# Performance work log

Measured on AMD Instinct MI355X. Metric: run time of the kernel, lower is better.

Reference implementation:

```python
import jax, jax.numpy as jnp
import numpy as np

B = 4096       # batch
D = 256        # num_features
H = 512        # proposal_hidden_units
K = 10         # mixture_components
C = 64         # context_units
L = 4          # proposal_residual_blocks
S = 10         # num_importance_samples (call default)
HEAD = 3 * K + C
LOG2PI = float(np.log(2.0 * np.pi))


def setup_inputs() -> dict:
    key = jax.random.key(0)
    ks = jax.random.split(key, 10)
    x = jax.random.normal(ks[0], (B, D), jnp.float32)
    observed_mask = (jax.random.uniform(ks[1], (B, D)) < 0.5).astype(jnp.float32)
    s_in = 1.0 / np.sqrt(2 * D)
    s_h = 1.0 / np.sqrt(H)
    W_in = (jax.random.normal(ks[2], (2 * D, H), jnp.float32) * s_in)
    b_in = jnp.zeros((H,), jnp.float32)
    W1 = jax.random.normal(ks[3], (L, H, H), jnp.float32) * s_h
    b1 = jnp.zeros((L, H), jnp.float32)
    W2 = jax.random.normal(ks[4], (L, H, H), jnp.float32) * s_h
    b2 = jnp.zeros((L, H), jnp.float32)
    W_fin = jax.random.normal(ks[5], (H, D * HEAD), jnp.float32) * s_h
    b_fin = jnp.zeros((D * HEAD,), jnp.float32)
    return {
        "x": x, "observed_mask": observed_mask,
        "W_in": W_in, "b_in": b_in,
        "W1": W1, "b1": b1, "W2": W2, "b2": b2,
        "W_fin": W_fin, "b_fin": b_fin,
        "num_importance_samples": S,
    }


def _proposal_params(x_o, observed_mask, W_in, b_in, W1, b1, W2, b2, W_fin, b_fin):
    # Residual MLP proposal network on [x_o, observed_mask].
    h = jnp.concatenate([x_o, observed_mask], axis=-1) @ W_in + b_in  # [B, H]
    for l in range(L):
        r = jax.nn.relu(h) @ W1[l] + b1[l]
        r = jax.nn.relu(r) @ W2[l] + b2[l]
        h = h + r
    out = (h @ W_fin + b_fin).reshape(h.shape[0], D, HEAD)  # [B, D, 3K+C]
    logits = out[..., :K]
    means = out[..., K:2 * K]
    scales = jax.nn.softplus(out[..., 2 * K:3 * K]) + 1e-3
    return logits, means, scales


def reference(x, observed_mask, W_in, b_in, W1, b1, W2, b2, W_fin, b_fin,
              num_importance_samples):
    query = 1.0 - observed_mask
    x_o = x * observed_mask
    x_u = x * query

    logits, means, scales = _proposal_params(
        x_o, observed_mask, W_in, b_in, W1, b1, W2, b2, W_fin, b_fin)

    # Per-feature mixture-of-Gaussians log-likelihood of x_u, masked by query.
    log_w = jax.nn.log_softmax(logits, axis=-1)               # [B, D, K]
    z = (x_u[..., None] - means) / scales
    comp_ll = -0.5 * z * z - jnp.log(scales) - 0.5 * LOG2PI   # [B, D, K]
    proposal_ll = jax.scipy.special.logsumexp(log_w + comp_ll, axis=-1) * query

    # Samples (stop_gradient in the original).
    skey = jax.random.key(1234)
    kc, kn = jax.random.split(skey)
    comp = jax.random.categorical(kc, logits, axis=-1,
                                  shape=(num_importance_samples,) + logits.shape[:2])  # [S, B, D]
    mu = jnp.take_along_axis(means[None], comp[..., None], axis=-1)[..., 0]    # [S, B, D]
    sg = jnp.take_along_axis(scales[None], comp[..., None], axis=-1)[..., 0]   # [S, B, D]
    eps = jax.random.normal(kn, comp.shape, jnp.float32)
    samples = mu + sg * eps                                   # [S, B, D]
    samples = jnp.transpose(samples, (1, 0, 2))               # [B, S, D]
    samples = jax.lax.stop_gradient(samples) * query[:, None, :]
    # call() multiplies by query twice (before and after selected_features block)
    proposal_samples = samples * query[:, None, :]

    proposal_mean = jnp.sum(jax.nn.softmax(logits, axis=-1) * means, axis=-1) * query
    proposal_mean = proposal_mean * query  # second masking, as in call()

    return proposal_ll, proposal_samples, proposal_mean
```

## Files before the change

kernel.cpp:

```cpp
#include <hip/hip_runtime.h>
#include <cstdint>

#define B 4096
#define D 256
#define H 512
#define K 10
#define NL 4
#define S 10
#define NOUT 30
#define HEADW 94
#define ND (B*D)
#define NFIN 7680
#define NLOG 2560
#define NMS  5120

typedef __bf16 bf16x8 __attribute__((ext_vector_type(8)));
typedef float  f32x16 __attribute__((ext_vector_type(16)));

__host__ __device__ inline void threefry2x32(uint32_t k0, uint32_t k1,
                                             uint32_t x0, uint32_t x1,
                                             uint32_t& o0, uint32_t& o1) {
  uint32_t ks2 = k0 ^ k1 ^ 0x1BD11BDAu;
#define TF_ROT(x, r) (((x) << (r)) | ((x) >> (32 - (r))))
#define TF_RND(r) { x0 += x1; x1 = TF_ROT(x1, r); x1 ^= x0; }
  x0 += k0; x1 += k1;
  TF_RND(13) TF_RND(15) TF_RND(26) TF_RND(6)
  x0 += k1; x1 += ks2 + 1u;
  TF_RND(17) TF_RND(29) TF_RND(16) TF_RND(24)
  x0 += ks2; x1 += k0 + 2u;
  TF_RND(13) TF_RND(15) TF_RND(26) TF_RND(6)
  x0 += k0; x1 += k1 + 3u;
  TF_RND(17) TF_RND(29) TF_RND(16) TF_RND(24)
  x0 += k1; x1 += ks2 + 4u;
  TF_RND(13) TF_RND(15) TF_RND(26) TF_RND(6)
  x0 += ks2; x1 += k0 + 5u;
  o0 = x0; o1 = x1;
#undef TF_RND
#undef TF_ROT
}

__device__ __forceinline__ uint32_t rb32(uint32_t k0, uint32_t k1, uint32_t idx) {
  uint32_t a, b;
  threefry2x32(k0, k1, 0u, idx, a, b);
  return a ^ b;
}

__device__ __forceinline__ float u01_from_bits(uint32_t bits) {
  return __uint_as_float((bits >> 9) | 0x3f800000u) - 1.0f;
}

__device__ __forceinline__ float erfinv_f32(float x) {
  float w = -log1pf(-x * x);
  float p;
  if (w < 5.0f) {
    w = w - 2.5f;
    p = 2.81022636e-08f;
    p = fmaf(p, w, 3.43273939e-07f);
    p = fmaf(p, w, -3.5233877e-06f);
    p = fmaf(p, w, -4.39150654e-06f);
    p = fmaf(p, w, 0.00021858087f);
    p = fmaf(p, w, -0.00125372503f);
    p = fmaf(p, w, -0.00417768164f);
    p = fmaf(p, w, 0.246640727f);
    p = fmaf(p, w, 1.50140941f);
  } else {
    w = sqrtf(w) - 3.0f;
    p = -0.000200214257f;
    p = fmaf(p, w, 0.000100950558f);
    p = fmaf(p, w, 0.00134934322f);
    p = fmaf(p, w, -0.00367342844f);
    p = fmaf(p, w, 0.00573950773f);
    p = fmaf(p, w, -0.0076224613f);
    p = fmaf(p, w, 0.00943887047f);
    p = fmaf(p, w, 1.00167406f);
    p = fmaf(p, w, 2.83297682f);
  }
  return p * x;
}

__device__ __forceinline__ unsigned short bf16_rne(float x) {
  uint32_t u = __float_as_uint(x);
  uint32_t r = u + 0x7fffu + ((u >> 16) & 1u);
  return (unsigned short)(r >> 16);
}

__device__ __forceinline__ void split2(float x, short& hi, short& lo) {
  unsigned short hb = bf16_rne(x);
  float hf = __uint_as_float((uint32_t)hb << 16);
  hi = (short)hb;
  lo = (short)bf16_rne(x - hf);
}

__device__ __forceinline__ void gload16(const void* g, void* l) {
  __builtin_amdgcn_global_load_lds(
      (const __attribute__((address_space(1))) void*)g,
      (__attribute__((address_space(3))) void*)l, 16, 0, 0);
}

template <int ROWS>
__device__ __forceinline__ void stage_region(const short* __restrict__ g,
                                             short* l, int wid, int lane) {
#pragma unroll
  for (int c = wid; c < ROWS / 16; c += 4) {
    const short* gp = g + (size_t)(c * 16 + (lane >> 2)) * 512 + (lane & 3) * 8;
    gload16(gp, l + c * 512);
  }
}

__global__ __launch_bounds__(256) void prep_kernel(const float* __restrict__ x,
                                                   const float* __restrict__ mask,
                                                   float* __restrict__ xcat) {
  int i = blockIdx.x * 256 + threadIdx.x;
  if (i >= B * 2 * D) return;
  int b = i >> 9, c = i & 511;
  float v = (c < D) ? x[b * D + c] * mask[b * D + c] : mask[b * D + (c - D)];
  xcat[i] = v;
}

__global__ __launch_bounds__(256) void wgatherL(const float* __restrict__ Wf,
                                                float* __restrict__ wsgL) {
  int c = blockIdx.x * 256 + threadIdx.x;
  int k = blockIdx.y;
  int dd = c / K, j = c - dd * K;
  wsgL[(size_t)k * NLOG + c] = Wf[(size_t)k * (D * HEADW) + dd * HEADW + j];
}

__global__ __launch_bounds__(256) void wsplit_ms(const float* __restrict__ Wf,
                                                 short* __restrict__ whi,
                                                 short* __restrict__ wlo) {
  __shared__ float tile[32][33];
  int n0 = blockIdx.x * 32, k0 = blockIdx.y * 32;
  int tx = threadIdx.x & 31, ty = threadIdx.x >> 5;
#pragma unroll
  for (int r = 0; r < 4; ++r) {
    int k = k0 + ty + r * 8;
    int n = n0 + tx;
    int dd = n / 20, j = n - dd * 20;
    tile[ty + r * 8][tx] = Wf[(size_t)k * (D * HEADW) + dd * HEADW + 10 + j];
  }
  __syncthreads();
#pragma unroll
  for (int r = 0; r < 4; ++r) {
    int n = n0 + ty + r * 8;
    int k = k0 + tx;
    float v = tile[tx][ty + r * 8];
    short hb, lb;
    split2(v, hb, lb);
    whi[(size_t)n * 512 + k] = hb;
    wlo[(size_t)n * 512 + k] = lb;
  }
}

template <int RELU, int RES>
__global__ __launch_bounds__(128) void gemm_trunk(const float* __restrict__ A,
                                                  const float* __restrict__ W,
                                                  const float* __restrict__ bias,
                                                  const float* res, float* C) {
  __shared__ float As[32 * 68];
  __shared__ float Ws[32 * 64];
  const int tid = threadIdx.x;
  const int lane = tid & 63, wid = tid >> 6;
  const int tx = tid & 15, ty = tid >> 4;
  const int bm = blockIdx.y * 64, bn = blockIdx.x * 64;
  const int ls = tid & 7, lm = tid >> 3;

  float acc[8][4] = {};

  for (int k0 = 0; k0 < H; k0 += 32) {
#pragma unroll
    for (int c = wid; c < 8; c += 2) {
      gload16(W + (size_t)(k0 + c * 4 + (lane >> 4)) * H + bn + (lane & 15) * 4,
              Ws + c * 256 + lane * 4);
    }
#pragma unroll
    for (int r = 0; r < 4; ++r) {
      int m = lm + 16 * r;
      float4 f = *(const float4*)(A + (size_t)(bm + m) * H + k0 + 4 * ls);
      if (RELU) {
        f.x = fmaxf(f.x, 0.0f); f.y = fmaxf(f.y, 0.0f);
        f.z = fmaxf(f.z, 0.0f); f.w = fmaxf(f.w, 0.0f);
      }
      As[(4 * ls + 0) * 68 + m] = f.x;
      As[(4 * ls + 1) * 68 + m] = f.y;
      As[(4 * ls + 2) * 68 + m] = f.z;
      As[(4 * ls + 3) * 68 + m] = f.w;
    }
    __syncthreads();
#pragma unroll
    for (int kk = 0; kk < 32; ++kk) {
      float a[8], b[4];
      *(float4*)(a + 0) = *(const float4*)(As + kk * 68 + ty * 8);
      *(float4*)(a + 4) = *(const float4*)(As + kk * 68 + ty * 8 + 4);
      *(float4*)(b + 0) = *(const float4*)(Ws + kk * 64 + tx * 4);
#pragma unroll
      for (int i = 0; i < 8; ++i)
#pragma unroll
        for (int j = 0; j < 4; ++j) acc[i][j] = fmaf(a[i], b[j], acc[i][j]);
    }
    __syncthreads();
  }
#pragma unroll
  for (int i = 0; i < 8; ++i) {
    int row = bm + ty * 8 + i;
#pragma unroll
    for (int j = 0; j < 4; ++j) {
      int col = bn + tx * 4 + j;
      float v = acc[i][j] + bias[col];
      if (RES) v = res[(size_t)row * H + col] + v;
      C[(size_t)row * H + col] = v;
    }
  }
}

__global__ __launch_bounds__(256) void gemm_logits(const float* __restrict__ A,
                                                   const float* __restrict__ Wg,
                                                   const float* __restrict__ bf,
                                                   float* __restrict__ headout) {
  __shared__ float As[32 * 136];
  __shared__ float Ws[32 * 128];
  const int tid = threadIdx.x;
  const int lane = tid & 63, wid = tid >> 6;
  const int tx = tid & 15, ty = tid >> 4;
  const int bm = blockIdx.y * 128, bn = blockIdx.x * 128;
  const int ls = tid & 7, lm = tid >> 3;

  float acc[8][8] = {};

  for (int k0 = 0; k0 < H; k0 += 32) {
#pragma unroll
    for (int c = wid; c < 16; c += 4) {
      gload16(Wg + (size_t)(k0 + c * 2 + (lane >> 5)) * NLOG + bn + (lane & 31) * 4,
              Ws + c * 256 + lane * 4);
    }
#pragma unroll
    for (int r = 0; r < 4; ++r) {
      int m = lm + 32 * r;
      float4 f = *(const float4*)(A + (size_t)(bm + m) * H + k0 + 4 * ls);
      As[(4 * ls + 0) * 136 + m] = f.x;
      As[(4 * ls + 1) * 136 + m] = f.y;
      As[(4 * ls + 2) * 136 + m] = f.z;
      As[(4 * ls + 3) * 136 + m] = f.w;
    }
    __syncthreads();
#pragma unroll
    for (int kk = 0; kk < 32; ++kk) {
      float a[8], b[8];
      *(float4*)(a + 0) = *(const float4*)(As + kk * 136 + ty * 8);
      *(float4*)(a + 4) = *(const float4*)(As + kk * 136 + ty * 8 + 4);
      *(float4*)(b + 0) = *(const float4*)(Ws + kk * 128 + tx * 8);
      *(float4*)(b + 4) = *(const float4*)(Ws + kk * 128 + tx * 8 + 4);
#pragma unroll
      for (int i = 0; i < 8; ++i)
#pragma unroll
        for (int j = 0; j < 8; ++j) acc[i][j] = fmaf(a[i], b[j], acc[i][j]);
    }
    __syncthreads();
  }
#pragma unroll
  for (int i = 0; i < 8; ++i) {
    int row = bm + ty * 8 + i;
#pragma unroll
    for (int j = 0; j < 8; ++j) {
      int c = bn + tx * 8 + j;
      int dd = c / K, jj = c - dd * K;
      float v = acc[i][j] + bf[dd * HEADW + jj];
      headout[(size_t)row * NFIN + dd * NOUT + jj] = v;
    }
  }
}

__global__ __launch_bounds__(256) void gemm_ms(const float* __restrict__ A,
                                               const short* __restrict__ Bh,
                                               const short* __restrict__ Bl,
                                               const float* __restrict__ bf,
                                               float* __restrict__ headout) {
  __shared__ short lds[4 * 128 * 32];
  const int tid = threadIdx.x;
  const int lane = tid & 63, wid = tid >> 6;
  const int wm = wid >> 1, wn = wid & 1;
  const int bm = blockIdx.y * 128, bn = blockIdx.x * 128;
  const int ls = tid & 7, lm = tid >> 3;

  short* ldsAh = lds;
  short* ldsAl = lds + 4096;
  short* ldsBh = lds + 8192;
  short* ldsBl = lds + 12288;

  const short* gBh = Bh + (size_t)bn * 512;
  const short* gBl = Bl + (size_t)bn * 512;

  f32x16 acc[2][2];
#pragma unroll
  for (int mt = 0; mt < 2; ++mt)
#pragma unroll
    for (int nt = 0; nt < 2; ++nt)
#pragma unroll
      for (int i = 0; i < 16; ++i) acc[mt][nt][i] = 0.0f;

  for (int k0 = 0; k0 < 512; k0 += 32) {
    stage_region<128>(gBh + k0, ldsBh, wid, lane);
    stage_region<128>(gBl + k0, ldsBl, wid, lane);
#pragma unroll
    for (int r = 0; r < 4; ++r) {
      int m = lm + 32 * r;
      float4 f = *(const float4*)(A + (size_t)(bm + m) * H + k0 + 4 * ls);
      short4 h4, l4;
      split2(f.x, h4.x, l4.x); split2(f.y, h4.y, l4.y);
      split2(f.z, h4.z, l4.z); split2(f.w, h4.w, l4.w);
      *(short4*)(ldsAh + m * 32 + 4 * ls) = h4;
      *(short4*)(ldsAl + m * 32 + 4 * ls) = l4;
    }
    __syncthreads();
#pragma unroll
    for (int sub = 0; sub < 2; ++sub) {
      bf16x8 ah[2], al[2], bh[2], bl[2];
#pragma unroll
      for (int mt = 0; mt < 2; ++mt) {
        int r = wm * 64 + mt * 32 + (lane & 31);
        int off = r * 32 + sub * 16 + (lane >> 5) * 8;
        ah[mt] = *(const bf16x8*)(ldsAh + off);
        al[mt] = *(const bf16x8*)(ldsAl + off);
      }
#pragma unroll
      for (int nt = 0; nt < 2; ++nt) {
        int r = wn * 64 + nt * 32 + (lane & 31);
        int off = r * 32 + sub * 16 + (lane >> 5) * 8;
        bh[nt] = *(const bf16x8*)(ldsBh + off);
        bl[nt] = *(const bf16x8*)(ldsBl + off);
      }
#pragma unroll
      for (int mt = 0; mt < 2; ++mt)
#pragma unroll
        for (int nt = 0; nt < 2; ++nt) {
          acc[mt][nt] = __builtin_amdgcn_mfma_f32_32x32x16_bf16(ah[mt], bh[nt], acc[mt][nt], 0, 0, 0);
          acc[mt][nt] = __builtin_amdgcn_mfma_f32_32x32x16_bf16(ah[mt], bl[nt], acc[mt][nt], 0, 0, 0);
          acc[mt][nt] = __builtin_amdgcn_mfma_f32_32x32x16_bf16(al[mt], bh[nt], acc[mt][nt], 0, 0, 0);
        }
    }
    __syncthreads();
  }

#pragma unroll
  for (int mt = 0; mt < 2; ++mt)
#pragma unroll
    for (int nt = 0; nt < 2; ++nt) {
      int col = bn + wn * 64 + nt * 32 + (lane & 31);
      int rbase = bm + wm * 64 + mt * 32 + 4 * (lane >> 5);
      int dd = col / 20, j = col - dd * 20;
#pragma unroll
      for (int reg = 0; reg < 16; ++reg) {
        int row = rbase + (reg & 3) + 8 * (reg >> 2);
        float v = acc[mt][nt][reg] + bf[dd * HEADW + 10 + j];
        if (j >= 10) v = (fmaxf(v, 0.0f) + log1pf(expf(-fabsf(v)))) + 0.001f;
        headout[(size_t)row * NFIN + dd * NOUT + 10 + j] = v;
      }
    }
}

__global__ __launch_bounds__(256) void init_counter(int* counter) {
  if (threadIdx.x == 0 && blockIdx.x == 0) *counter = 0;
}

__global__ __launch_bounds__(256) void compact_zero(const float* __restrict__ mask,
                                                    float* __restrict__ out_ll,
                                                    float* __restrict__ out_s,
                                                    float* __restrict__ out_mean,
                                                    int* __restrict__ list,
                                                    int* __restrict__ counter) {
  int idx = blockIdx.x * 256 + threadIdx.x;
  if (idx >= ND) return;
  if (mask[idx] != 0.0f) {
    int b = idx >> 8, d = idx & (D - 1);
    out_ll[idx] = 0.0f;
    out_mean[idx] = 0.0f;
#pragma unroll
    for (int s = 0; s < S; ++s) out_s[((size_t)b * S + s) * D + d] = 0.0f;
  } else {
    int pos = atomicAdd(counter, 1);
    list[pos] = idx;
  }
}

__global__ __launch_bounds__(256) void fused_tail(const float* __restrict__ head,
                                                  const float* __restrict__ x,
                                                  const float* __restrict__ mask,
                                                  const int* __restrict__ list,
                                                  const int* __restrict__ counter,
                                                  float* __restrict__ out_ll,
                                                  float* __restrict__ out_s,
                                                  float* __restrict__ out_mean,
                                                  uint32_t kc0, uint32_t kc1,
                                                  uint32_t kn0, uint32_t kn1) {
  int i = blockIdx.x * 256 + threadIdx.x;
  if (i >= *counter) return;
  int idx = list[i];
  int b = idx >> 8, d = idx & (D - 1);
  const float* hp = head + (size_t)idx * NOUT;
  float lg[K], mn[K], sc[K];
#pragma unroll
  for (int k = 0; k < K; ++k) { lg[k] = hp[k]; mn[k] = hp[K + k]; sc[k] = hp[2 * K + k]; }
  float q = 1.0f - mask[idx];
  float xu = x[idx] * q;
  float m = lg[0];
#pragma unroll
  for (int k = 1; k < K; ++k) m = fmaxf(m, lg[k]);
  float e[K];
  float sum = 0.0f;
#pragma unroll
  for (int k = 0; k < K; ++k) { e[k] = expf(lg[k] - m); sum += e[k]; }
  float lse = logf(sum);
  float a[K];
  float amax = -3.402823466e38f;
#pragma unroll
  for (int k = 0; k < K; ++k) {
    float z = (xu - mn[k]) / sc[k];
    float cll = -0.5f * z * z - logf(sc[k]) - 0.9189385332046727f;
    float lw = (lg[k] - m) - lse;
    a[k] = lw + cll;
    amax = fmaxf(amax, a[k]);
  }
  float s2 = 0.0f;
#pragma unroll
  for (int k = 0; k < K; ++k) s2 += expf(a[k] - amax);
  out_ll[idx] = (logf(s2) + amax) * q;
  float pm = 0.0f;
#pragma unroll
  for (int k = 0; k < K; ++k) pm += (e[k] / sum) * mn[k];
  out_mean[idx] = pm * q;
  float inv_e[K];
#pragma unroll
  for (int k = 0; k < K; ++k) inv_e[k] = 1.0f / e[k];
  for (int s = 0; s < S; ++s) {
    uint32_t t32 = (uint32_t)s * (uint32_t)ND + (uint32_t)idx;
    uint32_t base = t32 * (uint32_t)K;
    int best = 0;
    float rbest = 3.402823466e38f;
#pragma unroll
    for (int k = 0; k < K; ++k) {
      uint32_t bits = rb32(kc0, kc1, base + (uint32_t)k);
      float u = u01_from_bits(bits);
      float wv = -__log2f(u);
      float r = wv * inv_e[k];
      if (r < rbest) { rbest = r; best = k; }
    }
    uint32_t ebits = rb32(kn0, kn1, t32);
    float f = u01_from_bits(ebits);
    float r2 = f * 2.0f + (-0.99999994f);
    r2 = fmaxf(r2, -0.99999994f);
    float eps = 1.4142135623730951f * erfinv_f32(r2);
    out_s[((size_t)b * S + s) * D + d] = (mn[best] + sc[best] * eps) * q;
  }
}

extern "C" void kernel_launch(void* const* d_in, const int* in_sizes, int n_in,
                              void* d_out, int out_size, void* d_ws, size_t ws_size,
                              hipStream_t stream) {
  const float* x    = (const float*)d_in[0];
  const float* mask = (const float*)d_in[1];
  const float* W_in = (const float*)d_in[2];
  const float* b_in = (const float*)d_in[3];
  const float* W1   = (const float*)d_in[4];
  const float* b1   = (const float*)d_in[5];
  const float* W2   = (const float*)d_in[6];
  const float* b2   = (const float*)d_in[7];
  const float* Wf   = (const float*)d_in[8];
  const float* bf   = (const float*)d_in[9];

  char* w = (char*)d_ws;
  float* head   = (float*)w;
  float* xcat   = head;
  float* t      = head;
  float* h      = (float*)(w + 125829120);
  float* wsgL   = (float*)(w + 134217728);
  int*   list   = (int*)(w + 134217728);
  short* wms_h  = (short*)(w + 139460608);
  short* wms_l  = (short*)(w + 144703488);
  int*   counter = (int*)(w + 149946368);

  float* out_ll   = (float*)d_out;
  float* out_s    = out_ll + (size_t)ND;
  float* out_mean = out_s + (size_t)ND * S;

  wgatherL<<<dim3(NLOG / 256, 512), 256, 0, stream>>>(Wf, wsgL);
  wsplit_ms<<<dim3(NMS / 32, 512 / 32), 256, 0, stream>>>(Wf, wms_h, wms_l);

  prep_kernel<<<(B * 2 * D) / 256, 256, 0, stream>>>(x, mask, xcat);

  dim3 gtr(H / 64, B / 64);
  gemm_trunk<0, 0><<<gtr, 128, 0, stream>>>(xcat, W_in, b_in, nullptr, h);
  for (int l = 0; l < NL; ++l) {
    gemm_trunk<1, 0><<<gtr, 128, 0, stream>>>(h, W1 + (size_t)l * H * H,
                                              b1 + (size_t)l * H, nullptr, t);
    gemm_trunk<1, 1><<<gtr, 128, 0, stream>>>(t, W2 + (size_t)l * H * H,
                                              b2 + (size_t)l * H, h, h);
  }

  gemm_logits<<<dim3(NLOG / 128, B / 128), 256, 0, stream>>>(h, wsgL, bf, head);
  gemm_ms<<<dim3(NMS / 128, B / 128), 256, 0, stream>>>(h, wms_h, wms_l, bf, head);

  init_counter<<<1, 256, 0, stream>>>(counter);
  compact_zero<<<ND / 256, 256, 0, stream>>>(mask, out_ll, out_s, out_mean,
                                             list, counter);

  uint32_t kc0, kc1, kn0, kn1;
  threefry2x32(0u, 1234u, 0u, 0u, kc0, kc1);
  threefry2x32(0u, 1234u, 0u, 1u, kn0, kn1);
  fused_tail<<<ND / 256, 256, 0, stream>>>(head, x, mask, list, counter,
                                           out_ll, out_s, out_mean,
                                           kc0, kc1, kn0, kn1);
}
```

Before: 1.369 ms.

## Widen trunk GEMM blocks and merge logits/mixture head GEMMs into one launch

The trunk FP32 GEMM now uses 256 threads with a 64-deep K tile and 4x4 outputs per thread instead of 128 threads with 8x4, which doubles the waves per block and halves the number of K-loop synchronisations. The logits GEMM and the split-bf16 MFMA means/scales GEMM are fused into one kernel that branches on blockIdx.x and shares one LDS buffer. This removes a launch and lets both head workloads run concurrently to fill the GPU. The trade-off is more LDS per trunk block and fewer FMAs per LDS load.

```diff
diff --git a/kernel.cpp b/kernel.cpp
--- a/kernel.cpp
+++ b/kernel.cpp
@@ -152,23 +152,23 @@
 }
 
 template <int RELU, int RES>
-__global__ __launch_bounds__(128) void gemm_trunk(const float* __restrict__ A,
+__global__ __launch_bounds__(256) void gemm_trunk(const float* __restrict__ A,
                                                   const float* __restrict__ W,
                                                   const float* __restrict__ bias,
                                                   const float* res, float* C) {
-  __shared__ float As[32 * 68];
-  __shared__ float Ws[32 * 64];
+  __shared__ float As[64 * 68];
+  __shared__ float Ws[64 * 64];
   const int tid = threadIdx.x;
   const int lane = tid & 63, wid = tid >> 6;
   const int tx = tid & 15, ty = tid >> 4;
   const int bm = blockIdx.y * 64, bn = blockIdx.x * 64;
-  const int ls = tid & 7, lm = tid >> 3;
-
-  float acc[8][4] = {};
-
-  for (int k0 = 0; k0 < H; k0 += 32) {
-#pragma unroll
-    for (int c = wid; c < 8; c += 2) {
+  const int ls = tid & 15, lm = tid >> 4;
+
+  float acc[4][4] = {};
+
+  for (int k0 = 0; k0 < H; k0 += 64) {
+#pragma unroll
+    for (int c = wid; c < 16; c += 4) {
       gload16(W + (size_t)(k0 + c * 4 + (lane >> 4)) * H + bn + (lane & 15) * 4,
               Ws + c * 256 + lane * 4);
     }
@@ -187,21 +187,21 @@
     }
     __syncthreads();
 #pragma unroll
-    for (int kk = 0; kk < 32; ++kk) {
-      float a[8], b[4];
-      *(float4*)(a + 0) = *(const float4*)(As + kk * 68 + ty * 8);
-      *(float4*)(a + 4) = *(const float4*)(As + kk * 68 + ty * 8 + 4);
-      *(float4*)(b + 0) = *(const float4*)(Ws + kk * 64 + tx * 4);
-#pragma unroll
-      for (int i = 0; i < 8; ++i)
+    for (int kk = 0; kk < 64; ++kk) {
+      float4 a4 = *(const float4*)(As + kk * 68 + ty * 4);
+      float4 b4 = *(const float4*)(Ws + kk * 64 + tx * 4);
+      float a[4] = {a4.x, a4.y, a4.z, a4.w};
+      float b[4] = {b4.x, b4.y, b4.z, b4.w};
+#pragma unroll
+      for (int i = 0; i < 4; ++i)
 #pragma unroll
         for (int j = 0; j < 4; ++j) acc[i][j] = fmaf(a[i], b[j], acc[i][j]);
     }
     __syncthreads();
   }
 #pragma unroll
-  for (int i = 0; i < 8; ++i) {
-    int row = bm + ty * 8 + i;
+  for (int i = 0; i < 4; ++i) {
+    int row = bm + ty * 4 + i;
 #pragma unroll
     for (int j = 0; j < 4; ++j) {
       int col = bn + tx * 4 + j;
@@ -212,149 +212,148 @@
   }
 }
 
-__global__ __launch_bounds__(256) void gemm_logits(const float* __restrict__ A,
-                                                   const float* __restrict__ Wg,
-                                                   const float* __restrict__ bf,
-                                                   float* __restrict__ headout) {
-  __shared__ float As[32 * 136];
-  __shared__ float Ws[32 * 128];
+__global__ __launch_bounds__(256) void gemm_head(const float* __restrict__ A,
+                                                 const float* __restrict__ Wg,
+                                                 const short* __restrict__ Bh,
+                                                 const short* __restrict__ Bl,
+                                                 const float* __restrict__ bf,
+                                                 float* __restrict__ headout) {
+  __shared__ __align__(16) float smem[8448];
   const int tid = threadIdx.x;
   const int lane = tid & 63, wid = tid >> 6;
-  const int tx = tid & 15, ty = tid >> 4;
-  const int bm = blockIdx.y * 128, bn = blockIdx.x * 128;
-  const int ls = tid & 7, lm = tid >> 3;
-
-  float acc[8][8] = {};
-
-  for (int k0 = 0; k0 < H; k0 += 32) {
-#pragma unroll
-    for (int c = wid; c < 16; c += 4) {
-      gload16(Wg + (size_t)(k0 + c * 2 + (lane >> 5)) * NLOG + bn + (lane & 31) * 4,
-              Ws + c * 256 + lane * 4);
-    }
-#pragma unroll
-    for (int r = 0; r < 4; ++r) {
-      int m = lm + 32 * r;
-      float4 f = *(const float4*)(A + (size_t)(bm + m) * H + k0 + 4 * ls);
-      As[(4 * ls + 0) * 136 + m] = f.x;
-      As[(4 * ls + 1) * 136 + m] = f.y;
-      As[(4 * ls + 2) * 136 + m] = f.z;
-      As[(4 * ls + 3) * 136 + m] = f.w;
-    }
-    __syncthreads();
-#pragma unroll
-    for (int kk = 0; kk < 32; ++kk) {
-      float a[8], b[8];
-      *(float4*)(a + 0) = *(const float4*)(As + kk * 136 + ty * 8);
-      *(float4*)(a + 4) = *(const float4*)(As + kk * 136 + ty * 8 + 4);
-      *(float4*)(b + 0) = *(const float4*)(Ws + kk * 128 + tx * 8);
-      *(float4*)(b + 4) = *(const float4*)(Ws + kk * 128 + tx * 8 + 4);
-#pragma unroll
-      for (int i = 0; i < 8; ++i)
-#pragma unroll
-        for (int j = 0; j < 8; ++j) acc[i][j] = fmaf(a[i], b[j], acc[i][j]);
-    }
-    __syncthreads();
-  }
-#pragma unroll
-  for (int i = 0; i < 8; ++i) {
-    int row = bm + ty * 8 + i;
-#pragma unroll
-    for (int j = 0; j < 8; ++j) {
-      int c = bn + tx * 8 + j;
-      int dd = c / K, jj = c - dd * K;
-      float v = acc[i][j] + bf[dd * HEADW + jj];
-      headout[(size_t)row * NFIN + dd * NOUT + jj] = v;
-    }
-  }
-}
-
-__global__ __launch_bounds__(256) void gemm_ms(const float* __restrict__ A,
-                                               const short* __restrict__ Bh,
-                                               const short* __restrict__ Bl,
-                                               const float* __restrict__ bf,
-                                               float* __restrict__ headout) {
-  __shared__ short lds[4 * 128 * 32];
-  const int tid = threadIdx.x;
-  const int lane = tid & 63, wid = tid >> 6;
-  const int wm = wid >> 1, wn = wid & 1;
-  const int bm = blockIdx.y * 128, bn = blockIdx.x * 128;
-  const int ls = tid & 7, lm = tid >> 3;
-
-  short* ldsAh = lds;
-  short* ldsAl = lds + 4096;
-  short* ldsBh = lds + 8192;
-  short* ldsBl = lds + 12288;
-
-  const short* gBh = Bh + (size_t)bn * 512;
-  const short* gBl = Bl + (size_t)bn * 512;
-
-  f32x16 acc[2][2];
-#pragma unroll
-  for (int mt = 0; mt < 2; ++mt)
-#pragma unroll
-    for (int nt = 0; nt < 2; ++nt)
-#pragma unroll
-      for (int i = 0; i < 16; ++i) acc[mt][nt][i] = 0.0f;
-
-  for (int k0 = 0; k0 < 512; k0 += 32) {
-    stage_region<128>(gBh + k0, ldsBh, wid, lane);
-    stage_region<128>(gBl + k0, ldsBl, wid, lane);
-#pragma unroll
-    for (int r = 0; r < 4; ++r) {
-      int m = lm + 32 * r;
-      float4 f = *(const float4*)(A + (size_t)(bm + m) * H + k0 + 4 * ls);
-      short4 h4, l4;
-      split2(f.x, h4.x, l4.x); split2(f.y, h4.y, l4.y);
-      split2(f.z, h4.z, l4.z); split2(f.w, h4.w, l4.w);
-      *(short4*)(ldsAh + m * 32 + 4 * ls) = h4;
-      *(short4*)(ldsAl + m * 32 + 4 * ls) = l4;
-    }
-    __syncthreads();
-#pragma unroll
-    for (int sub = 0; sub < 2; ++sub) {
-      bf16x8 ah[2], al[2], bh[2], bl[2];
-#pragma unroll
-      for (int mt = 0; mt < 2; ++mt) {
-        int r = wm * 64 + mt * 32 + (lane & 31);
-        int off = r * 32 + sub * 16 + (lane >> 5) * 8;
-        ah[mt] = *(const bf16x8*)(ldsAh + off);
-        al[mt] = *(const bf16x8*)(ldsAl + off);
-      }
+  const int bm = blockIdx.y * 128;
+
+  if (blockIdx.x < 20) {
+    float* As = smem;
+    float* Ws = smem + 4352;
+    const int tx = tid & 15, ty = tid >> 4;
+    const int bn = blockIdx.x * 128;
+    const int ls = tid & 7, lm = tid >> 3;
+
+    float acc[8][8] = {};
+
+    for (int k0 = 0; k0 < H; k0 += 32) {
+#pragma unroll
+      for (int c = wid; c < 16; c += 4) {
+        gload16(Wg + (size_t)(k0 + c * 2 + (lane >> 5)) * NLOG + bn + (lane & 31) * 4,
+                Ws + c * 256 + lane * 4);
+      }
+#pragma unroll
+      for (int r = 0; r < 4; ++r) {
+        int m = lm + 32 * r;
+        float4 f = *(const float4*)(A + (size_t)(bm + m) * H + k0 + 4 * ls);
+        As[(4 * ls + 0) * 136 + m] = f.x;
+        As[(4 * ls + 1) * 136 + m] = f.y;
+        As[(4 * ls + 2) * 136 + m] = f.z;
+        As[(4 * ls + 3) * 136 + m] = f.w;
+      }
+      __syncthreads();
+#pragma unroll
+      for (int kk = 0; kk < 32; ++kk) {
+        float a[8], b[8];
+        *(float4*)(a + 0) = *(const float4*)(As + kk * 136 + ty * 8);
+        *(float4*)(a + 4) = *(const float4*)(As + kk * 136 + ty * 8 + 4);
+        *(float4*)(b + 0) = *(const float4*)(Ws + kk * 128 + tx * 8);
+        *(float4*)(b + 4) = *(const float4*)(Ws + kk * 128 + tx * 8 + 4);
+#pragma unroll
+        for (int i = 0; i < 8; ++i)
+#pragma unroll
+          for (int j = 0; j < 8; ++j) acc[i][j] = fmaf(a[i], b[j], acc[i][j]);
+      }
+      __syncthreads();
+    }
+#pragma unroll
+    for (int i = 0; i < 8; ++i) {
+      int row = bm + ty * 8 + i;
+#pragma unroll
+      for (int j = 0; j < 8; ++j) {
+        int c = bn + tx * 8 + j;
+        int dd = c / K, jj = c - dd * K;
+        float v = acc[i][j] + bf[dd * HEADW + jj];
+        headout[(size_t)row * NFIN + dd * NOUT + jj] = v;
+      }
+    }
+  } else {
+    short* lds = (short*)smem;
+    const int wm = wid >> 1, wn = wid & 1;
+    const int bn = (blockIdx.x - 20) * 128;
+    const int ls = tid & 7, lm = tid >> 3;
+
+    short* ldsAh = lds;
+    short* ldsAl = lds + 4096;
+    short* ldsBh = lds + 8192;
+    short* ldsBl = lds + 12288;
+
+    const short* gBh = Bh + (size_t)bn * 512;
+    const short* gBl = Bl + (size_t)bn * 512;
+
+    f32x16 acc[2][2];
+#pragma unroll
+    for (int mt = 0; mt < 2; ++mt)
+#pragma unroll
+      for (int nt = 0; nt < 2; ++nt)
+#pragma unroll
+        for (int i = 0; i < 16; ++i) acc[mt][nt][i] = 0.0f;
+
+    for (int k0 = 0; k0 < 512; k0 += 32) {
+      stage_region<128>(gBh + k0, ldsBh, wid, lane);
+      stage_region<128>(gBl + k0, ldsBl, wid, lane);
+#pragma unroll
+      for (int r = 0; r < 4; ++r) {
+        int m = lm + 32 * r;
+        float4 f = *(const float4*)(A + (size_t)(bm + m) * H + k0 + 4 * ls);
+        short4 h4, l4;
+        split2(f.x, h4.x, l4.x); split2(f.y, h4.y, l4.y);
+        split2(f.z, h4.z, l4.z); split2(f.w, h4.w, l4.w);
+        *(short4*)(ldsAh + m * 32 + 4 * ls) = h4;
+        *(short4*)(ldsAl + m * 32 + 4 * ls) = l4;
+      }
+      __syncthreads();
+#pragma unroll
+      for (int sub = 0; sub < 2; ++sub) {
+        bf16x8 ah[2], al[2], bh[2], bl[2];
+#pragma unroll
+        for (int mt = 0; mt < 2; ++mt) {
+          int r = wm * 64 + mt * 32 + (lane & 31);
+          int off = r * 32 + sub * 16 + (lane >> 5) * 8;
+          ah[mt] = *(const bf16x8*)(ldsAh + off);
+          al[mt] = *(const bf16x8*)(ldsAl + off);
+        }
+#pragma unroll
+        for (int nt = 0; nt < 2; ++nt) {
+          int r = wn * 64 + nt * 32 + (lane & 31);
+          int off = r * 32 + sub * 16 + (lane >> 5) * 8;
+          bh[nt] = *(const bf16x8*)(ldsBh + off);
+          bl[nt] = *(const bf16x8*)(ldsBl + off);
+        }
+#pragma unroll
+        for (int mt = 0; mt < 2; ++mt)
+#pragma unroll
+          for (int nt = 0; nt < 2; ++nt) {
+            acc[mt][nt] = __builtin_amdgcn_mfma_f32_32x32x16_bf16(ah[mt], bh[nt], acc[mt][nt], 0, 0, 0);
+            acc[mt][nt] = __builtin_amdgcn_mfma_f32_32x32x16_bf16(ah[mt], bl[nt], acc[mt][nt], 0, 0, 0);
+            acc[mt][nt] = __builtin_amdgcn_mfma_f32_32x32x16_bf16(al[mt], bh[nt], acc[mt][nt], 0, 0, 0);
+          }
+      }
+      __syncthreads();
+    }
+
+#pragma unroll
+    for (int mt = 0; mt < 2; ++mt)
 #pragma unroll
       for (int nt = 0; nt < 2; ++nt) {
-        int r = wn * 64 + nt * 32 + (lane & 31);
-        int off = r * 32 + sub * 16 + (lane >> 5) * 8;
-        bh[nt] = *(const bf16x8*)(ldsBh + off);
-        bl[nt] = *(const bf16x8*)(ldsBl + off);
-      }
-#pragma unroll
-      for (int mt = 0; mt < 2; ++mt)
-#pragma unroll
-        for (int nt = 0; nt < 2; ++nt) {
-          acc[mt][nt] = __builtin_amdgcn_mfma_f32_32x32x16_bf16(ah[mt], bh[nt], acc[mt][nt], 0, 0, 0);
-          acc[mt][nt] = __builtin_amdgcn_mfma_f32_32x32x16_bf16(ah[mt], bl[nt], acc[mt][nt], 0, 0, 0);
-          acc[mt][nt] = __builtin_amdgcn_mfma_f32_32x32x16_bf16(al[mt], bh[nt], acc[mt][nt], 0, 0, 0);
+        int col = bn + wn * 64 + nt * 32 + (lane & 31);
+        int rbase = bm + wm * 64 + mt * 32 + 4 * (lane >> 5);
+        int dd = col / 20, j = col - dd * 20;
+#pragma unroll
+        for (int reg = 0; reg < 16; ++reg) {
+          int row = rbase + (reg & 3) + 8 * (reg >> 2);
+          float v = acc[mt][nt][reg] + bf[dd * HEADW + 10 + j];
+          if (j >= 10) v = (fmaxf(v, 0.0f) + log1pf(expf(-fabsf(v)))) + 0.001f;
+          headout[(size_t)row * NFIN + dd * NOUT + 10 + j] = v;
         }
-    }
-    __syncthreads();
-  }
-
-#pragma unroll
-  for (int mt = 0; mt < 2; ++mt)
-#pragma unroll
-    for (int nt = 0; nt < 2; ++nt) {
-      int col = bn + wn * 64 + nt * 32 + (lane & 31);
-      int rbase = bm + wm * 64 + mt * 32 + 4 * (lane >> 5);
-      int dd = col / 20, j = col - dd * 20;
-#pragma unroll
-      for (int reg = 0; reg < 16; ++reg) {
-        int row = rbase + (reg & 3) + 8 * (reg >> 2);
-        float v = acc[mt][nt][reg] + bf[dd * HEADW + 10 + j];
-        if (j >= 10) v = (fmaxf(v, 0.0f) + log1pf(expf(-fabsf(v)))) + 0.001f;
-        headout[(size_t)row * NFIN + dd * NOUT + 10 + j] = v;
-      }
-    }
+      }
+  }
 }
 
 __global__ __launch_bounds__(256) void init_counter(int* counter) {
@@ -487,16 +486,15 @@
   prep_kernel<<<(B * 2 * D) / 256, 256, 0, stream>>>(x, mask, xcat);
 
   dim3 gtr(H / 64, B / 64);
-  gemm_trunk<0, 0><<<gtr, 128, 0, stream>>>(xcat, W_in, b_in, nullptr, h);
+  gemm_trunk<0, 0><<<gtr, 256, 0, stream>>>(xcat, W_in, b_in, nullptr, h);
   for (int l = 0; l < NL; ++l) {
-    gemm_trunk<1, 0><<<gtr, 128, 0, stream>>>(h, W1 + (size_t)l * H * H,
+    gemm_trunk<1, 0><<<gtr, 256, 0, stream>>>(h, W1 + (size_t)l * H * H,
                                               b1 + (size_t)l * H, nullptr, t);
-    gemm_trunk<1, 1><<<gtr, 128, 0, stream>>>(t, W2 + (size_t)l * H * H,
+    gemm_trunk<1, 1><<<gtr, 256, 0, stream>>>(t, W2 + (size_t)l * H * H,
                                               b2 + (size_t)l * H, h, h);
   }
 
-  gemm_logits<<<dim3(NLOG / 128, B / 128), 256, 0, stream>>>(h, wsgL, bf, head);
-  gemm_ms<<<dim3(NMS / 128, B / 128), 256, 0, stream>>>(h, wms_h, wms_l, bf, head);
+  gemm_head<<<dim3(60, B / 128), 256, 0, stream>>>(h, wsgL, wms_h, wms_l, bf, head);
 
   init_counter<<<1, 256, 0, stream>>>(counter);
   compact_zero<<<ND / 256, 256, 0, stream>>>(mask, out_ll, out_s, out_mean,
```

Result: faster. 1.213 ms (-11.4%).
